# Optimization experiments

Hardware: AMD Instinct MI355X
Metric: run time of the kernel (lower is better)

Reference implementation:

```python
import jax, jax.numpy as jnp
import numpy as np
from jax.scipy.linalg import cholesky, solve_triangular, cho_solve

N, M, D = 16384, 2048, 8
VAR, LS = 1.0, 0.5      # RBF kernel hyperparameters (same for kernel_f and kernel_g)
JITTER = 1e-6
BATCH_RATE = 1.0
HALF_LOG_2PI = 0.5 * float(np.log(2.0 * np.pi))


def rbf(x1, x2):
    # K[i,j] = VAR * exp(-||x1_i - x2_j||^2 / (2 LS^2))
    d2 = (jnp.sum(x1 * x1, 1)[:, None] + jnp.sum(x2 * x2, 1)[None, :]
          - 2.0 * (x1 @ x2.T))
    return VAR * jnp.exp(-0.5 * d2 / (LS * LS))


def setup_inputs() -> dict:
    key = jax.random.key(0)
    ks = jax.random.split(key, 7)
    x = jax.random.normal(ks[0], (N, D), dtype=jnp.float32)
    y = jax.random.normal(ks[1], (N, 1), dtype=jnp.float32)
    z = 2.0 * jax.random.uniform(ks[2], (M, D), dtype=jnp.float32) - 1.0  # inducing inputs in [-1,1]^D
    q_m_f = 0.5 * jax.random.normal(ks[3], (M, 1), dtype=jnp.float32)
    q_m_g = 0.5 * jax.random.normal(ks[4], (M, 1), dtype=jnp.float32)
    # Cholesky-like params: identity plus small strictly-lower noise -> PD covariance
    q_L_f = jnp.eye(M, dtype=jnp.float32) + 0.01 * jnp.tril(
        jax.random.normal(ks[5], (M, M), dtype=jnp.float32), -1)
    q_L_g = jnp.eye(M, dtype=jnp.float32) + 0.01 * jnp.tril(
        jax.random.normal(ks[6], (M, M), dtype=jnp.float32), -1)
    return {"x": x, "y": y, "z": z, "q_m_f": q_m_f, "q_L_f": q_L_f,
            "q_m_g": q_m_g, "q_L_g": q_L_g}


def _gp_marginals_and_kl(x, z, q_m, q_L_raw):
    """Marginal posterior mean/var at x and KL(q(u)||p(u)) for one sparse GP."""
    L_S = jnp.tril(q_L_raw)                     # [M,M]
    Kuu = rbf(z, z) + JITTER * jnp.eye(M, dtype=x.dtype)
    Lk = cholesky(Kuu, lower=True)
    Kfu = rbf(x, z)                             # [N,M]
    # A = Kfu @ Kuu^{-1}
    A = cho_solve((Lk, True), Kfu.T).T          # [N,M]
    m = (A @ q_m)[:, 0]                         # [N]
    # diag(Kff + A (S - Kuu) A^T) = diag(Kff) + diag(A S A^T) - diag(Kfu A^T)
    S = L_S @ L_S.T
    diag_Kff = jnp.full((x.shape[0],), VAR, dtype=x.dtype)
    v = diag_Kff + jnp.sum((A @ S) * A, axis=1) - jnp.sum(A * Kfu, axis=1)
    # KL(N(q_m, S) || N(0, Kuu))
    alpha = solve_triangular(Lk, q_m, lower=True)       # Kuu^{-1/2} m
    W = solve_triangular(Lk, L_S, lower=True)           # Kuu^{-1/2} L_S
    logdet_K = 2.0 * jnp.sum(jnp.log(jnp.diag(Lk)))
    logdet_S = 2.0 * jnp.sum(jnp.log(jnp.abs(jnp.diag(L_S))))
    kl = 0.5 * (jnp.sum(W * W) + jnp.sum(alpha * alpha)
                - jnp.asarray(M, x.dtype) + logdet_K - logdet_S)
    return m, v, kl


def reference(x, y, z, q_m_f, q_L_f, q_m_g, q_L_g):
    m_f, v_f, kl_f = _gp_marginals_and_kl(x, z, q_m_f, q_L_f)
    m_g, v_g, kl_g = _gp_marginals_and_kl(x, z, q_m_g, q_L_g)
    yv = y[:, 0]
    # HetGaussian variational expectation (Saul et al. 2016):
    # E_q[log N(y | f, exp(g))] per point
    expectation = (-HALF_LOG_2PI - 0.5 * m_g
                   - 0.5 * ((yv - m_f) ** 2 + v_f) * jnp.exp(-m_g + 0.5 * v_g))
    elbo = BATCH_RATE * jnp.sum(expectation) - (kl_f + kl_g)
    return -elbo
```

## Files before the change

### kernel.cpp

```cpp
#include <hip/hip_runtime.h>
#include <math.h>

#define NN 16384
#define MM 2048
#define DD 8
#define NB 32
#define SZB ((size_t)16777216)

constexpr float HLOG2PI = 0.91893853320467274178f;

using short8  = __attribute__((ext_vector_type(8))) short;
using float4v = __attribute__((ext_vector_type(4))) float;

__device__ __forceinline__ float4v f4zero(){ float4v v; v[0]=0.f; v[1]=0.f; v[2]=0.f; v[3]=0.f; return v; }

__device__ __forceinline__ void bfsplit(float v, short& h, short& lo){
  unsigned b = __float_as_uint(v);
  h = (short)(b >> 16);
  float hf = __uint_as_float(b & 0xFFFF0000u);
  lo = (short)(__float_as_uint(v - hf) >> 16);
}
__device__ __forceinline__ float bf2f(short s){
  return __uint_as_float(((unsigned)(unsigned short)s) << 16);
}
__device__ __forceinline__ float4v mfma3(short8 ah, short8 al, short8 bh, short8 bl, float4v c){
  c = __builtin_amdgcn_mfma_f32_16x16x32_bf16(ah, bh, c, 0, 0, 0);
  c = __builtin_amdgcn_mfma_f32_16x16x32_bf16(ah, bl, c, 0, 0, 0);
  c = __builtin_amdgcn_mfma_f32_16x16x32_bf16(al, bh, c, 0, 0, 0);
  return c;
}

__device__ __forceinline__ float block_reduce(float v, float* scratch){
  int lane = threadIdx.x & 63;
  int w    = threadIdx.x >> 6;
  #pragma unroll
  for (int off=32; off; off>>=1) v += __shfl_down(v, off, 64);
  __syncthreads();
  if (lane==0) scratch[w] = v;
  __syncthreads();
  float r = 0.f;
  if (threadIdx.x < 4) r = scratch[threadIdx.x];
  if (w==0){ r += __shfl_down(r, 2, 64); r += __shfl_down(r, 1, 64); }
  return r;
}

__device__ __forceinline__ void stage64(float (*S)[68], const float* __restrict__ g, int ld, int t){
  #pragma unroll
  for (int p=t; p<1024; p+=256)
    *(float4*)&S[p>>4][(p&15)*4] = *(const float4*)&g[(size_t)(p>>4)*ld + (p&15)*4];
}
__device__ __forceinline__ void tile_gemm_step(float acc[4][4], const float (*As)[68], const float (*Bs)[68], int tx, int ty){
  for (int k=0;k<64;++k){
    float ar[4], bc4[4];
    #pragma unroll
    for (int u=0;u<4;++u){ ar[u]=As[ty*4+u][k]; bc4[u]=Bs[k][tx*4+u]; }
    #pragma unroll
    for (int u=0;u<4;++u)
      #pragma unroll
      for (int v=0;v<4;++v) acc[u][v] += ar[u]*bc4[v];
  }
}
__device__ __forceinline__ void tile_syrk_step(float acc[4][4], const float (*P)[68], const float (*Q)[68], int tx, int ty){
  for (int k=0;k<64;++k){
    float pr[4], qc[4];
    #pragma unroll
    for (int u=0;u<4;++u){ pr[u]=P[ty*4+u][k]; qc[u]=Q[tx*4+u][k]; }
    #pragma unroll
    for (int u=0;u<4;++u)
      #pragma unroll
      for (int v=0;v<4;++v) acc[u][v] += pr[u]*qc[v];
  }
}

__device__ __forceinline__ void factor64_reg(const float (*S)[68],
    float* __restrict__ lkd, float* __restrict__ sdg_, int d, int t){
  if (t < 64){
    float xr[64];
    #pragma unroll
    for (int c4=0;c4<16;++c4) *(float4*)&xr[c4*4] = *(const float4*)&S[t][c4*4];
    float myrp = 1.f;
    #pragma unroll
    for (int j=0;j<64;++j){
      float ajj = __shfl(xr[j], j, 64);
      float piv = sqrtf(fmaxf(ajj, 1e-20f));
      float rp  = 1.f/piv;
      float val = xr[j]*rp;
      if (t==j){ xr[j] = piv; myrp = rp; }
      else if (t>j) xr[j] = val;
      else val = 0.f;
      #pragma unroll
      for (int c=j+1;c<64;++c){
        float vc = __shfl(val, c, 64);
        if (c<=t) xr[c] -= val*vc;
      }
    }
    #pragma unroll
    for (int c=0;c<64;++c) if (c>t) xr[c] = 0.f;
    #pragma unroll
    for (int c4=0;c4<16;++c4)
      *(float4*)&lkd[d*4096 + t*64 + c4*4] = *(float4*)&xr[c4*4];
    sdg_[d*64 + t] = myrp;
  }
}


__global__ __launch_bounds__(256) void phase0_kernel(
    const float* __restrict__ z, float* __restrict__ kuu){
  __shared__ float As[64][68];
  __shared__ float Bs[64][68];
  const int t = threadIdx.x, tx = t & 15, ty = t >> 4;
  int idx = blockIdx.x;
  int r=0; while ((r+1)*(r+2)/2 <= idx) ++r;
  int c = idx - r*(r+1)/2;
  for (int p=t; p<128; p+=256){ int i=p>>1, h=p&1;
    *(float4*)&As[i][h*4] = *(const float4*)&z[(size_t)(r*64+i)*DD + h*4];
    *(float4*)&Bs[i][h*4] = *(const float4*)&z[(size_t)(c*64+i)*DD + h*4]; }
  __syncthreads();
  #pragma unroll
  for (int u=0;u<4;++u){
    float4 o;
    float* ov = (float*)&o;
    #pragma unroll
    for (int v=0;v<4;++v){
      float d2=0.f;
      #pragma unroll
      for (int d=0;d<8;++d){ float df=As[ty*4+u][d]-Bs[tx*4+v][d]; d2+=df*df; }
      float val = __expf(-2.f*d2);
      if (r*64+ty*4+u == c*64+tx*4+v) val += 1e-6f;
      ov[v] = val;
    }
    *(float4*)&kuu[(size_t)(r*64+ty*4+u)*MM + c*64 + tx*4] = o;
  }
}

__global__ __launch_bounds__(256) void diag0_kernel(
    const float* __restrict__ kuu, float* __restrict__ lkdiag, float* __restrict__ sdg){
  __shared__ float As[64][68];
  const int t = threadIdx.x;
  stage64(As, kuu, MM, t);
  __syncthreads();
  factor64_reg(As, lkdiag, sdg, 0, t);
}

__global__ __launch_bounds__(256) void panel_kernel(
    float* __restrict__ kuu, float* __restrict__ lkdiag,
    float* __restrict__ sdg, float* __restrict__ ltri, int kb){
  __shared__ float As[64][68];
  __shared__ float Bs[64][68];
  __shared__ float Cs[64][68];
  __shared__ float sd[64];
  const int t = threadIdx.x, tx = t & 15, ty = t >> 4;
  int idx = blockIdx.x;
  int r=0; while ((r+1)*(r+2)/2 <= idx) ++r;
  int c = idx - r*(r+1)/2;
  int bi = kb+1+r, bc = kb+1+c;
  stage64(Cs, lkdiag + kb*4096, 64, t);
  if (t < 64) sd[t] = sdg[kb*64 + t];
  stage64(As, kuu + (size_t)(bi*64)*MM + kb*64, MM, t);
  if (bc != bi) stage64(Bs, kuu + (size_t)(bc*64)*MM + kb*64, MM, t);
  __syncthreads();
  {
    int w = t>>6, l = t&63;
    if (w==0 || (w==1 && bc!=bi)){
      float (*S)[68] = (w==0)? As : Bs;
      float xr[64];
      #pragma unroll
      for (int c4=0;c4<16;++c4) *(float4*)&xr[c4*4] = *(const float4*)&S[l][c4*4];
      #pragma unroll
      for (int j=0;j<64;++j){
        float xj = xr[j]*sd[j];
        xr[j] = xj;
        #pragma unroll
        for (int cc=j+1;cc<64;++cc) xr[cc] -= xj*Cs[cc][j];
      }
      #pragma unroll
      for (int c4=0;c4<16;++c4) *(float4*)&S[l][c4*4] = *(float4*)&xr[c4*4];
    }
  }
  __syncthreads();
  if (bc == kb+1){
    for (int p=t;p<1024;p+=256)
      *(float4*)&ltri[(size_t)(bi*64+(p>>4))*MM + kb*64 + (p&15)*4] =
          *(float4*)&As[p>>4][(p&15)*4];
  }
  float acc[4][4] = {};
  tile_syrk_step(acc, As, (bc==bi)? As : Bs, tx, ty);
  if (bi==kb+1 && bc==kb+1){
    __syncthreads();
    #pragma unroll
    for (int u=0;u<4;++u)
      #pragma unroll
      for (int v=0;v<4;++v) Bs[ty*4+u][tx*4+v] = acc[u][v];
    __syncthreads();
    for (int p=t;p<1024;p+=256){
      int i=p>>4, c4=p&15;
      float4 kv = *(const float4*)&kuu[(size_t)(bi*64+i)*MM + bi*64 + c4*4];
      float4 bv = *(float4*)&Bs[i][c4*4];
      float4 o; o.x=kv.x-bv.x; o.y=kv.y-bv.y; o.z=kv.z-bv.z; o.w=kv.w-bv.w;
      *(float4*)&As[i][c4*4] = o;
    }
    __syncthreads();
    factor64_reg(As, lkdiag, sdg, kb+1, t);
  } else {
    #pragma unroll
    for (int u=0;u<4;++u){
      float4* dst = (float4*)&kuu[(size_t)(bi*64+ty*4+u)*MM + bc*64 + tx*4];
      float4 o = *dst;
      o.x-=acc[u][0]; o.y-=acc[u][1]; o.z-=acc[u][2]; o.w-=acc[u][3];
      *dst = o;
    }
  }
}

__global__ __launch_bounds__(256) void phase2_kernel(
    const float* __restrict__ lkdiag, float* __restrict__ linv){
  __shared__ float As[64][68];
  __shared__ float Bs[64][68];
  const int t = threadIdx.x, bid = blockIdx.x;
  stage64(As, lkdiag + bid*4096, 64, t);
  __syncthreads();
  if (t < 64){
    for (int j=0;j<64;++j){
      float s = (j==t)?1.f:0.f;
      for (int k=t;k<j;++k) s -= As[j][k]*Bs[k][t];
      Bs[j][t] = (j>=t)? s/As[j][j] : 0.f;
    }
  }
  __syncthreads();
  for (int p=t;p<1024;p+=256){ int i=p>>4, c4=p&15;
    *(float4*)&linv[(size_t)(bid*64+i)*MM + bid*64 + c4*4] = *(float4*)&Bs[i][c4*4]; }
}

__global__ __launch_bounds__(256) void p3l0_kernel(
    const float* __restrict__ ltri, float* __restrict__ linv){
  __shared__ float As[64][68];
  __shared__ float Bs[64][68];
  const int t = threadIdx.x, tx = t & 15, ty = t >> 4;
  int m = blockIdx.x;
  stage64(As, ltri + (size_t)((2*m+1)*64)*MM + (2*m)*64, MM, t);
  stage64(Bs, linv + (size_t)((2*m)*64)*MM   + (2*m)*64, MM, t);
  __syncthreads();
  float acc[4][4]={};
  tile_gemm_step(acc, As, Bs, tx, ty);
  __syncthreads();
  #pragma unroll
  for (int u=0;u<4;++u)
    #pragma unroll
    for (int v=0;v<4;++v) Bs[ty*4+u][tx*4+v] = acc[u][v];
  stage64(As, linv + (size_t)((2*m+1)*64)*MM + (2*m+1)*64, MM, t);
  __syncthreads();
  float o[4][4]={};
  tile_gemm_step(o, As, Bs, tx, ty);
  #pragma unroll
  for (int u=0;u<4;++u)
    *(float4*)&linv[(size_t)((2*m+1)*64+ty*4+u)*MM + (2*m)*64 + tx*4] =
        make_float4(-o[u][0],-o[u][1],-o[u][2],-o[u][3]);
}

__global__ __launch_bounds__(256) void p3l1_kernel(
    const float* __restrict__ ltri, float* __restrict__ linv, float* __restrict__ ptmp){
  __shared__ float As[64][68];
  __shared__ float Bs[64][68];
  const int t = threadIdx.x, tx = t & 15, ty = t >> 4;
  int m = blockIdx.x;
  float* pm = ptmp + (size_t)m*128*128;
  for (int ti=0; ti<2; ++ti)
    for (int tj=0; tj<2; ++tj){
      int rb = m*4 + 2 + ti, cb0 = m*4;
      float acc[4][4]={};
      for (int k=tj; k<2; ++k){
        __syncthreads();
        stage64(As, ltri + (size_t)(rb*64)*MM + (cb0+k)*64, MM, t);
        stage64(Bs, linv + (size_t)((cb0+k)*64)*MM + (cb0+tj)*64, MM, t);
        __syncthreads();
        tile_gemm_step(acc, As, Bs, tx, ty);
      }
      #pragma unroll
      for (int u=0;u<4;++u)
        *(float4*)&pm[(size_t)(ti*64+ty*4+u)*128 + tj*64 + tx*4] =
            make_float4(acc[u][0],acc[u][1],acc[u][2],acc[u][3]);
    }
  for (int ti=0; ti<2; ++ti)
    for (int tj=0; tj<2; ++tj){
      int rb = m*4 + 2 + ti;
      float acc[4][4]={};
      for (int k=0; k<=ti; ++k){
        __syncthreads();
        stage64(As, linv + (size_t)(rb*64)*MM + (m*4+2+k)*64, MM, t);
        stage64(Bs, pm + (size_t)(k*64)*128 + tj*64, 128, t);
        __syncthreads();
        tile_gemm_step(acc, As, Bs, tx, ty);
      }
      #pragma unroll
      for (int u=0;u<4;++u)
        *(float4*)&linv[(size_t)(rb*64+ty*4+u)*MM + (m*4+tj)*64 + tx*4] =
            make_float4(-acc[u][0],-acc[u][1],-acc[u][2],-acc[u][3]);
    }
}

__global__ __launch_bounds__(256) void p3lA_kernel(
    const float* __restrict__ ltri, const float* __restrict__ linv,
    float* __restrict__ ptmp, int s){
  __shared__ float As[64][68];
  __shared__ float Bs[64][68];
  const int t = threadIdx.x, tx = t & 15, ty = t >> 4;
  int nb = 1<<s, b = 64<<s;
  float* pmb = ptmp + (s==2 ? 131072 : (s==3 ? 393216 : 917504));
  int idx = blockIdx.x;
  int m = idx/(nb*nb), r2 = idx%(nb*nb);
  int ti = r2/nb, tj = r2%nb;
  int rb = m*2*nb + nb + ti, cb0 = m*2*nb;
  float acc[4][4]={};
  for (int k=tj; k<nb; ++k){
    __syncthreads();
    stage64(As, ltri + (size_t)(rb*64)*MM + (cb0+k)*64, MM, t);
    stage64(Bs, linv + (size_t)((cb0+k)*64)*MM + (cb0+tj)*64, MM, t);
    __syncthreads();
    tile_gemm_step(acc, As, Bs, tx, ty);
  }
  float* pm = pmb + (size_t)m*b*b;
  #pragma unroll
  for (int u=0;u<4;++u)
    *(float4*)&pm[(size_t)(ti*64+ty*4+u)*b + tj*64 + tx*4] =
        make_float4(acc[u][0],acc[u][1],acc[u][2],acc[u][3]);
}

__global__ __launch_bounds__(256) void p3lB_kernel(
    float* __restrict__ linv, const float* __restrict__ ptmp, int s){
  __shared__ float As[64][68];
  __shared__ float Bs[64][68];
  const int t = threadIdx.x, tx = t & 15, ty = t >> 4;
  int nb = 1<<s, b = 64<<s;
  const float* pmb = ptmp + (s==2 ? 131072 : (s==3 ? 393216 : 917504));
  int idx = blockIdx.x;
  int m = idx/(nb*nb), r2 = idx%(nb*nb);
  int ti = r2/nb, tj = r2%nb;
  int rb = m*2*nb + nb + ti;
  const float* pm = pmb + (size_t)m*b*b;
  float acc[4][4]={};
  for (int k=0; k<=ti; ++k){
    __syncthreads();
    stage64(As, linv + (size_t)(rb*64)*MM + (m*2*nb+nb+k)*64, MM, t);
    stage64(Bs, pm + (size_t)(k*64)*b + tj*64, b, t);
    __syncthreads();
    tile_gemm_step(acc, As, Bs, tx, ty);
  }
  #pragma unroll
  for (int u=0;u<4;++u)
    *(float4*)&linv[(size_t)(rb*64+ty*4+u)*MM + (m*2*nb+tj)*64 + tx*4] =
        make_float4(-acc[u][0],-acc[u][1],-acc[u][2],-acc[u][3]);
}

__global__ __launch_bounds__(256) void w_kernel(
    const float* __restrict__ linv, const float* __restrict__ qlf,
    const float* __restrict__ qlg, float* __restrict__ wf, float* __restrict__ wg){
  __shared__ float As[64][68];
  __shared__ float Bs[64][68];
  const int t = threadIdx.x, tx = t & 15, ty = t >> 4;
  int idx = blockIdx.x;
  int gp = idx/528, rem = idx%528;
  int bi=0; while ((bi+1)*(bi+2)/2 <= rem) ++bi;
  int bj = rem - bi*(bi+1)/2;
  const float* ql = gp ? qlg : qlf;
  float* w        = gp ? wg  : wf;
  float acc[4][4]={};
  for (int bk=bj; bk<=bi; ++bk){
    __syncthreads();
    stage64(As, linv + (size_t)(bi*64)*MM + bk*64, MM, t);
    stage64(Bs, ql   + (size_t)(bk*64)*MM + bj*64, MM, t);
    __syncthreads();
    if (bk==bj){
      for (int p=t;p<4096;p+=256){ int i=p>>6, c=p&63; if (i<c) Bs[i][c]=0.f; }
      __syncthreads();
    }
    tile_gemm_step(acc, As, Bs, tx, ty);
  }
  #pragma unroll
  for (int u=0;u<4;++u)
    *(float4*)&w[(size_t)(bi*64+ty*4+u)*MM + bj*64 + tx*4] =
        make_float4(acc[u][0],acc[u][1],acc[u][2],acc[u][3]);
}

__global__ __launch_bounds__(256) void alpha_kernel(
    const float* __restrict__ linv, const float* __restrict__ qmf,
    const float* __restrict__ qmg, float* __restrict__ af, float* __restrict__ ag){
  int t = threadIdx.x;
  int gw = blockIdx.x*4 + (t>>6), l = t&63;
  for (int job=gw; job<4096; job+=1024){
    int gp = job>>11, r = job&2047;
    const float* qm = gp ? qmg : qmf;
    float s=0.f;
    for (int c=l; c<=r; c+=64) s += linv[(size_t)r*MM+c]*qm[c];
    #pragma unroll
    for (int off=32; off; off>>=1) s += __shfl_down(s, off, 64);
    if (l==0) (gp ? ag : af)[r] = s;
  }
}


__global__ __launch_bounds__(256) void zfrag_kernel(const float* __restrict__ z,
    short* __restrict__ zfh, short* __restrict__ zfl, float* __restrict__ zn2){
  int zr = blockIdx.x*256 + threadIdx.x;
  float v[DD]; float s = 0.f;
  #pragma unroll
  for (int d=0; d<DD; ++d){ v[d] = z[zr*DD + d]; s += v[d]*v[d]; }
  zn2[zr] = s;
  size_t base = (size_t)(zr >> 4)*512 + (zr & 15)*32;
  #pragma unroll
  for (int k=0; k<32; ++k){
    short h = 0, lo = 0;
    if (k < DD) bfsplit(v[k], h, lo);
    zfh[base + k] = h; zfl[base + k] = lo;
  }
}

__global__ __launch_bounds__(256) void red_small(const float* __restrict__ lkd,
    const float* __restrict__ qlf, const float* __restrict__ qlg,
    const float* __restrict__ af, const float* __restrict__ ag,
    float* __restrict__ scal){
  __shared__ float scratch[4];
  float ldk=0, ldf=0, ldg=0, a2f=0, a2g=0;
  for (int i=threadIdx.x;i<MM;i+=256){
    int kb = i>>6, r = i&63;
    ldk += __logf(lkd[kb*4096 + r*64 + r]);
    ldf += __logf(fabsf(qlf[(size_t)i*MM+i]));
    ldg += __logf(fabsf(qlg[(size_t)i*MM+i]));
    float v = af[i]; a2f += v*v;
    v = ag[i];       a2g += v*v;
  }
  float r;
  r = block_reduce(ldk, scratch); if (threadIdx.x==0) scal[0] = 2.f*r;
  r = block_reduce(ldf, scratch); if (threadIdx.x==0) scal[1] = 2.f*r;
  r = block_reduce(ldg, scratch); if (threadIdx.x==0) scal[2] = 2.f*r;
  r = block_reduce(a2f, scratch); if (threadIdx.x==0) scal[3] = r;
  r = block_reduce(a2g, scratch); if (threadIdx.x==0) scal[4] = r;
}

__global__ __launch_bounds__(256) void redw_kernel(const float* __restrict__ wf,
    const float* __restrict__ wg, float* __restrict__ scal){
  __shared__ float scratch[4];
  size_t start  = (size_t)blockIdx.x*256 + threadIdx.x;
  size_t stride = (size_t)gridDim.x*256;
  float sf=0, sg=0;
  for (size_t p=start;p<(size_t)MM*MM;p+=stride){
    float v=wf[p]; sf += v*v;
    v=wg[p];       sg += v*v;
  }
  float r = block_reduce(sf, scratch);
  if (threadIdx.x==0) atomicAdd(&scal[5], r);
  r = block_reduce(sg, scratch);
  if (threadIdx.x==0) atomicAdd(&scal[6], r);
}

__global__ void kl_kernel(const float* __restrict__ scal, float* __restrict__ out){
  float klf = 0.5f*(scal[5] + scal[3] - (float)MM + scal[0] - scal[1]);
  float klg = 0.5f*(scal[6] + scal[4] - (float)MM + scal[0] - scal[2]);
  out[0] += klf + klg;
}

__global__ __launch_bounds__(256) void split_rowmajor(const float* __restrict__ src,
    short* __restrict__ dh, short* __restrict__ dl){
  int p = blockIdx.x*256 + threadIdx.x;
  int chunk = p >> 9, wi = p & 511;
  int mo = chunk >> 6, ko = chunk & 63;
  int row = mo*16 + (wi >> 5), col = ko*32 + (wi & 31);
  float v = src[(size_t)row*MM + col];
  short h, lo; bfsplit(v, h, lo);
  dh[p] = h; dl[p] = lo;
}

__global__ __launch_bounds__(256) void split_transpose(const float* __restrict__ src,
    short* __restrict__ dh, short* __restrict__ dl){
  __shared__ float tile[32][33];
  int t = threadIdx.x;
  int mb = blockIdx.x, kb = blockIdx.y;
  #pragma unroll
  for (int k=0;k<4;++k){
    int idx = t + k*256;
    int lr = idx >> 5, lc = idx & 31;
    tile[lr][lc] = src[(size_t)(kb*32+lr)*MM + mb*32 + lc];
  }
  __syncthreads();
  #pragma unroll
  for (int e=0;e<4;++e){
    int p = t*4 + e;
    int c = p >> 9, wi = p & 511;
    int i = (wi >> 5) & 15, kk = wi & 31;
    float v = tile[kk][c*16 + i];
    short h, lo; bfsplit(v, h, lo);
    size_t gp = ((size_t)(mb*2 + c)*64 + kb)*512 + wi;
    dh[gp] = h; dl[gp] = lo;
  }
}

__global__ __launch_bounds__(256, 2) void tt_mfma(
    const float* __restrict__ x, const float* __restrict__ zn2,
    const short* __restrict__ zfh, const short* __restrict__ zfl,
    const short* __restrict__ lvh, const short* __restrict__ lvl,
    short* __restrict__ tth, short* __restrict__ ttl){
  __shared__ __align__(16) short lAh[8192], lAl[8192], lBh[8192], lBl[8192];
  int t = threadIdx.x;
  int l = t & 63, w = t >> 6;
  int istrip = blockIdx.x, bj2 = blockIdx.y;
  int li = l & 15, q = l >> 4;
  int lofs = li*32 + q*8;
  int wn4 = (w>>1)*4, wm4 = (w&1)*4;

  short8 xh[2], xl[2];
  float xn2v[8];
  {
    float xn2t[2];
    #pragma unroll
    for (int tn=0; tn<2; ++tn){
      int n = istrip*128 + w*32 + tn*16 + li;
      const float4* xp = (const float4*)(x + (size_t)n*DD);
      float4 p0 = xp[0], p1 = xp[1];
      float v[8] = {p0.x,p0.y,p0.z,p0.w,p1.x,p1.y,p1.z,p1.w};
      float s = 0.f;
      #pragma unroll
      for (int d=0; d<8; ++d) s += v[d]*v[d];
      xn2t[tn] = s;
      short8 hh, ll;
      #pragma unroll
      for (int j=0; j<8; ++j){
        short h=0, lo=0;
        if (q==0) bfsplit(v[j], h, lo);
        hh[j]=h; ll[j]=lo;
      }
      xh[tn]=hh; xl[tn]=ll;
    }
    #pragma unroll
    for (int tn=0; tn<2; ++tn)
      #pragma unroll
      for (int r=0; r<4; ++r)
        xn2v[tn*4+r] = __shfl(xn2t[tn], q*4 + r, 64);
  }

  float4v acc[4][4];
  #pragma unroll
  for (int i=0;i<4;++i)
    #pragma unroll
    for (int j=0;j<4;++j) acc[i][j] = f4zero();

  int nkt = 2*bj2 + 2;
  for (int bk=0; bk<nkt; ++bk){
    __syncthreads();
    {
      short8 zh[4], zl[4];
      float zt2[4];
      #pragma unroll
      for (int tz=0; tz<4; ++tz){
        size_t zo = (size_t)(bk*4 + tz)*512 + lofs;
        zh[tz] = *(const short8*)(zfh + zo);
        zl[tz] = *(const short8*)(zfl + zo);
        zt2[tz] = zn2[bk*64 + tz*16 + li];
      }
      #pragma unroll
      for (int tn=0; tn<2; ++tn){
        #pragma unroll
        for (int tz=0; tz<4; ++tz){
          float4v s4 = mfma3(xh[tn], xl[tn], zh[tz], zl[tz], f4zero());
          #pragma unroll
          for (int r=0; r<4; ++r){
            float e = __expf(4.f*s4[r] - 2.f*(xn2v[tn*4+r] + zt2[tz]));
            short h, lo; bfsplit(e, h, lo);
            int pos = ((w*2+tn)*2 + (tz>>1))*512 + (q*4+r)*32 + (tz&1)*16 + li;
            lAh[pos] = h; lAl[pos] = lo;
          }
        }
      }
    }
    #pragma unroll
    for (int c4 = t; c4 < 1024; c4 += 256){
      int ch = c4 >> 6, wdi = c4 & 63;
      size_t g = ((size_t)(bj2*8 + (ch>>1))*64 + (size_t)(bk*2 + (ch&1)))*64 + wdi;
      ((uint4*)lBh)[c4] = ((const uint4*)lvh)[g];
      ((uint4*)lBl)[c4] = ((const uint4*)lvl)[g];
    }
    __syncthreads();
    #pragma unroll
    for (int s=0; s<2; ++s){
      short8 ah[4], al[4], bh[4], bl[4];
      #pragma unroll
      for (int tn=0; tn<4; ++tn){
        int off = ((wn4+tn)*2 + s)*512 + lofs;
        ah[tn] = *(const short8*)&lAh[off];
        al[tn] = *(const short8*)&lAl[off];
      }
      #pragma unroll
      for (int tm=0; tm<4; ++tm){
        int off = ((wm4+tm)*2 + s)*512 + lofs;
        bh[tm] = *(const short8*)&lBh[off];
        bl[tm] = *(const short8*)&lBl[off];
      }
      #pragma unroll
      for (int tn=0; tn<4; ++tn)
        #pragma unroll
        for (int tm=0; tm<4; ++tm)
          acc[tn][tm] = mfma3(ah[tn], al[tn], bh[tm], bl[tm], acc[tn][tm]);
    }
  }
  #pragma unroll
  for (int tn=0; tn<4; ++tn){
    int no_g = istrip*8 + wn4 + tn;
    #pragma unroll
    for (int tm=0; tm<4; ++tm){
      int mo_g = bj2*4 + (w&1)*2 + (tm>>1);
      size_t cb = ((size_t)no_g*64 + mo_g)*512;
      #pragma unroll
      for (int r=0; r<4; ++r){
        short h, lo; bfsplit(acc[tn][tm][r], h, lo);
        size_t pos = cb + (q*4+r)*32 + (tm&1)*16 + li;
        tth[pos] = h; ttl[pos] = lo;
      }
    }
  }
}

__global__ __launch_bounds__(256) void lin_v2(const short* __restrict__ tth,
    const short* __restrict__ ttl, const float* __restrict__ af, const float* __restrict__ ag,
    float* __restrict__ t2, float* __restrict__ lf, float* __restrict__ lg){
  int t = threadIdx.x;
  int w = t >> 6, l = t & 63;
  int n = blockIdx.x*4 + w;
  int g = l >> 2, j = l & 3;
  float s2=0.f, sf=0.f, sg=0.f;
  #pragma unroll
  for (int it=0; it<4; ++it){
    int ck = g + it*16;
    size_t off = ((size_t)(n>>4)*64 + ck)*512 + (n&15)*32 + j*8;
    short8 h8 = *(const short8*)(tth + off);
    short8 l8 = *(const short8*)(ttl + off);
    int m0 = ck*32 + j*8;
    float4 a0 = *(const float4*)(af + m0), a1 = *(const float4*)(af + m0 + 4);
    float4 g0 = *(const float4*)(ag + m0), g1 = *(const float4*)(ag + m0 + 4);
    float av[8] = {a0.x,a0.y,a0.z,a0.w,a1.x,a1.y,a1.z,a1.w};
    float gv[8] = {g0.x,g0.y,g0.z,g0.w,g1.x,g1.y,g1.z,g1.w};
    #pragma unroll
    for (int e=0; e<8; ++e){
      float tv = bf2f(h8[e]) + bf2f(l8[e]);
      s2 += tv*tv; sf += tv*av[e]; sg += tv*gv[e];
    }
  }
  #pragma unroll
  for (int off=32; off; off>>=1){
    s2 += __shfl_down(s2, off, 64);
    sf += __shfl_down(sf, off, 64);
    sg += __shfl_down(sg, off, 64);
  }
  if (l==0){ t2[n] = s2; lf[n] = sf; lg[n] = sg; }
}

__global__ __launch_bounds__(256, 2) void quad_mfma(
    const short* __restrict__ tth, const short* __restrict__ ttl,
    const short* __restrict__ wfh, const short* __restrict__ wfl,
    const short* __restrict__ wgh, const short* __restrict__ wgl,
    float* __restrict__ vfq, float* __restrict__ vgq){
  __shared__ __align__(16) short lAh[8192], lAl[8192], lBh[8192], lBl[8192];
  int t = threadIdx.x, l = t & 63, w = t >> 6;
  int istrip = blockIdx.x, bj2 = blockIdx.y;
  const short* gbh = blockIdx.z ? wgh : wfh;
  const short* gbl = blockIdx.z ? wgl : wfl;
  float* vq = blockIdx.z ? vgq : vfq;
  int li = l & 15, q = l >> 4;
  int lofs = li*32 + q*8;
  int wn4 = (w>>1)*4, wm4 = (w&1)*4;

  float4v acc[4][4];
  #pragma unroll
  for (int i=0;i<4;++i)
    #pragma unroll
    for (int j=0;j<4;++j) acc[i][j] = f4zero();

  for (int bk=2*bj2; bk<32; ++bk){
    __syncthreads();
    #pragma unroll
    for (int c4 = t; c4 < 1024; c4 += 256){
      int ch = c4 >> 6, wdi = c4 & 63;
      size_t ga = ((size_t)(istrip*8 + (ch>>1))*64 + (size_t)(bk*2 + (ch&1)))*64 + wdi;
      ((uint4*)lAh)[c4] = ((const uint4*)tth)[ga];
      ((uint4*)lAl)[c4] = ((const uint4*)ttl)[ga];
      size_t gb = ((size_t)(bj2*8 + (ch>>1))*64 + (size_t)(bk*2 + (ch&1)))*64 + wdi;
      ((uint4*)lBh)[c4] = ((const uint4*)gbh)[gb];
      ((uint4*)lBl)[c4] = ((const uint4*)gbl)[gb];
    }
    __syncthreads();
    #pragma unroll
    for (int s=0; s<2; ++s){
      short8 ah[4], al[4], bh[4], bl[4];
      #pragma unroll
      for (int tn=0; tn<4; ++tn){
        int off = ((wn4+tn)*2 + s)*512 + lofs;
        ah[tn] = *(const short8*)&lAh[off];
        al[tn] = *(const short8*)&lAl[off];
      }
      #pragma unroll
      for (int tm=0; tm<4; ++tm){
        int off = ((wm4+tm)*2 + s)*512 + lofs;
        bh[tm] = *(const short8*)&lBh[off];
        bl[tm] = *(const short8*)&lBl[off];
      }
      #pragma unroll
      for (int tn=0; tn<4; ++tn)
        #pragma unroll
        for (int tm=0; tm<4; ++tm)
          acc[tn][tm] = mfma3(ah[tn], al[tn], bh[tm], bl[tm], acc[tn][tm]);
    }
  }
  float rs[16];
  #pragma unroll
  for (int tn=0; tn<4; ++tn)
    #pragma unroll
    for (int r=0; r<4; ++r){
      float s = 0.f;
      #pragma unroll
      for (int tm=0; tm<4; ++tm){ float v = acc[tn][tm][r]; s += v*v; }
      rs[tn*4+r] = s;
    }
  #pragma unroll
  for (int off=8; off; off>>=1)
    #pragma unroll
    for (int k=0; k<16; ++k) rs[k] += __shfl_down(rs[k], off, 16);
  if (li == 0){
    #pragma unroll
    for (int tn=0; tn<4; ++tn)
      #pragma unroll
      for (int r=0; r<4; ++r){
        int n = istrip*128 + (w>>1)*64 + tn*16 + q*4 + r;
        atomicAdd(&vq[n], rs[tn*4+r]);
      }
  }
}

__global__ __launch_bounds__(256) void final_kernel(const float* __restrict__ y,
    const float* __restrict__ t2, const float* __restrict__ lf, const float* __restrict__ lg,
    const float* __restrict__ vfq, const float* __restrict__ vgq, float* __restrict__ out){
  __shared__ float scratch[4];
  int i = blockIdx.x*256 + threadIdx.x;
  float mf = lf[i], mg = lg[i];
  float vf = 1.f + vfq[i] - t2[i];
  float vg = 1.f + vgq[i] - t2[i];
  float dy = y[i] - mf;
  float e = -HLOG2PI - 0.5f*mg - 0.5f*(dy*dy + vf)*__expf(-mg + 0.5f*vg);
  float r = block_reduce(e, scratch);
  if (threadIdx.x==0) atomicAdd(out, -r);
}

extern "C" void kernel_launch(void* const* d_in, const int* in_sizes, int n_in,
                              void* d_out, int out_size, void* d_ws, size_t ws_size,
                              hipStream_t stream){
  (void)in_sizes; (void)n_in; (void)out_size; (void)ws_size;
  const float* x   = (const float*)d_in[0];
  const float* y   = (const float*)d_in[1];
  const float* z   = (const float*)d_in[2];
  const float* qmf = (const float*)d_in[3];
  const float* qlf = (const float*)d_in[4];
  const float* qmg = (const float*)d_in[5];
  const float* qlg = (const float*)d_in[6];
  float* out = (float*)d_out;
  char* Bw = (char*)d_ws;

  float* kuu  = (float*)Bw;
  float* linv = (float*)(Bw + SZB);
  float* wf   = (float*)(Bw + 2*SZB);
  float* wg   = (float*)(Bw + 3*SZB);
  short* lvh  = (short*)Bw;
  short* lvl  = (short*)(Bw + SZB/2);
  short* wfh  = (short*)(Bw + SZB);
  short* wfl  = (short*)(Bw + SZB + SZB/2);
  short* wgh  = (short*)(Bw + 2*SZB);
  short* wgl  = (short*)(Bw + 2*SZB + SZB/2);
  short* tth  = (short*)(Bw + 3*SZB);
  short* ttl  = (short*)(Bw + 3*SZB + (size_t)NN*MM*2);
  float* ltri   = (float*)(Bw + 4*SZB);
  float* ptmp   = (float*)(Bw + 5*SZB);
  float* lkdiag = (float*)(Bw + 5*SZB + (size_t)8388608);
  float* sdg    = (float*)(Bw + 5*SZB + (size_t)8388608 + (size_t)524288);
  float* sm   = (float*)(Bw + 3*SZB + (size_t)NN*MM*4);
  float* af = sm;          float* ag = af + MM;
  float* t2 = ag + MM;     float* lf = t2 + NN;   float* lg = lf + NN;
  float* vfq = lg + NN;    float* vgq = vfq + NN; float* scal = vgq + NN;
  float* zn2 = scal + 64 + 2048;
  short* zfh = (short*)(zn2 + MM);
  short* zfl = zfh + MM*32;

  hipMemsetAsync(out, 0, sizeof(float), stream);
  hipMemsetAsync(vfq, 0, (size_t)(2*NN + 64 + 2048)*sizeof(float), stream);
  hipMemsetAsync(wf,  0, 2*SZB, stream);
  hipMemsetAsync(linv,0, SZB,   stream);

  zfrag_kernel<<<MM/256, 256, 0, stream>>>(z, zfh, zfl, zn2);

  phase0_kernel<<<528, 256, 0, stream>>>(z, kuu);
  diag0_kernel<<<1, 256, 0, stream>>>(kuu, lkdiag, sdg);
  for (int kb = 0; kb < 31; ++kb){
    int T = NB - 1 - kb;
    panel_kernel<<<T*(T+1)/2, 256, 0, stream>>>(kuu, lkdiag, sdg, ltri, kb);
  }
  phase2_kernel<<<NB, 256, 0, stream>>>(lkdiag, linv);
  p3l0_kernel<<<16, 256, 0, stream>>>(ltri, linv);
  p3l1_kernel<<<8, 256, 0, stream>>>(ltri, linv, ptmp);
  for (int s = 2; s < 5; ++s){
    int nb = 1<<s, mc = 16>>s;
    p3lA_kernel<<<mc*nb*nb, 256, 0, stream>>>(ltri, linv, ptmp, s);
    p3lB_kernel<<<mc*nb*nb, 256, 0, stream>>>(linv, ptmp, s);
  }
  w_kernel<<<2*528, 256, 0, stream>>>(linv, qlf, qlg, wf, wg);
  alpha_kernel<<<256, 256, 0, stream>>>(linv, qmf, qmg, af, ag);

  red_small<<<1, 256, 0, stream>>>(lkdiag, qlf, qlg, af, ag, scal);
  redw_kernel<<<512, 256, 0, stream>>>(wf, wg, scal);
  kl_kernel<<<1, 1, 0, stream>>>(scal, out);

  split_rowmajor<<<MM*MM/256, 256, 0, stream>>>(linv, lvh, lvl);
  split_transpose<<<dim3(MM/32, MM/32), 256, 0, stream>>>(wf, wfh, wfl);
  split_transpose<<<dim3(MM/32, MM/32), 256, 0, stream>>>(wg, wgh, wgl);

  tt_mfma<<<dim3(NN/128, MM/128), 256, 0, stream>>>(x, zn2, zfh, zfl, lvh, lvl, tth, ttl);
  lin_v2<<<NN/4, 256, 0, stream>>>(tth, ttl, af, ag, t2, lf, lg);
  quad_mfma<<<dim3(NN/128, MM/128, 2), 256, 0, stream>>>(tth, ttl, wfh, wfl, wgh, wgl, vfq, vgq);
  final_kernel<<<NN/256, 256, 0, stream>>>(y, t2, lf, lg, vfq, vgq, out);
}
```

Before: 3.914 ms.

## Swizzle LDS tiles in MFMA GEMMs and merge split kernels into one launch

Measured after the change: 3.875 ms. Within noise of the previous version (-1.0%).

```diff
diff --git a/kernel.cpp b/kernel.cpp
--- a/kernel.cpp
+++ b/kernel.cpp
@@ -458,22 +458,31 @@
   out[0] += klf + klg;
 }
 
-__global__ __launch_bounds__(256) void split_rowmajor(const float* __restrict__ src,
-    short* __restrict__ dh, short* __restrict__ dl){
-  int p = blockIdx.x*256 + threadIdx.x;
-  int chunk = p >> 9, wi = p & 511;
-  int mo = chunk >> 6, ko = chunk & 63;
-  int row = mo*16 + (wi >> 5), col = ko*32 + (wi & 31);
-  float v = src[(size_t)row*MM + col];
-  short h, lo; bfsplit(v, h, lo);
-  dh[p] = h; dl[p] = lo;
-}
-
-__global__ __launch_bounds__(256) void split_transpose(const float* __restrict__ src,
-    short* __restrict__ dh, short* __restrict__ dl){
+__global__ __launch_bounds__(256) void split_all(
+    const float* __restrict__ linv, const float* __restrict__ wf,
+    const float* __restrict__ wg, short* __restrict__ lvh, short* __restrict__ lvl,
+    short* __restrict__ wfh, short* __restrict__ wfl,
+    short* __restrict__ wgh, short* __restrict__ wgl){
   __shared__ float tile[32][33];
-  int t = threadIdx.x;
-  int mb = blockIdx.x, kb = blockIdx.y;
+  const int t = threadIdx.x;
+  const int bid = blockIdx.x;
+  if (bid < 16384){
+    int p = bid*256 + t;
+    int chunk = p >> 9, wi = p & 511;
+    int mo = chunk >> 6, ko = chunk & 63;
+    int row = mo*16 + (wi >> 5), col = ko*32 + (wi & 31);
+    float v = linv[(size_t)row*MM + col];
+    short h, lo; bfsplit(v, h, lo);
+    lvh[p] = h; lvl[p] = lo;
+    return;
+  }
+  int idx2 = bid - 16384;
+  int zz = idx2 >> 12;
+  int rem = idx2 & 4095;
+  int mb = rem & 63, kb = rem >> 6;
+  const float* src = zz ? wg : wf;
+  short* dh = zz ? wgh : wfh;
+  short* dl = zz ? wgl : wfl;
   #pragma unroll
   for (int k=0;k<4;++k){
     int idx = t + k*256;
@@ -504,6 +513,7 @@
   int istrip = blockIdx.x, bj2 = blockIdx.y;
   int li = l & 15, q = l >> 4;
   int lofs = li*32 + q*8;
+  int lofs_s = li*32 + ((q ^ ((li>>1)&3)))*8;
   int wn4 = (w>>1)*4, wm4 = (w&1)*4;
 
   short8 xh[2], xl[2];
@@ -564,7 +574,9 @@
           for (int r=0; r<4; ++r){
             float e = __expf(4.f*s4[r] - 2.f*(xn2v[tn*4+r] + zt2[tz]));
             short h, lo; bfsplit(e, h, lo);
-            int pos = ((w*2+tn)*2 + (tz>>1))*512 + (q*4+r)*32 + (tz&1)*16 + li;
+            int rowc = q*4 + r;
+            int slot2 = (((tz&1)*2 + (li>>3)) ^ ((rowc>>1)&3));
+            int pos = ((w*2+tn)*2 + (tz>>1))*512 + rowc*32 + slot2*8 + (li&7);
             lAh[pos] = h; lAl[pos] = lo;
           }
         }
@@ -573,9 +585,11 @@
     #pragma unroll
     for (int c4 = t; c4 < 1024; c4 += 256){
       int ch = c4 >> 6, wdi = c4 & 63;
+      int wsw = (wdi & 60) | ((wdi ^ (wdi >> 3)) & 3);
+      int dst = ch*64 + wsw;
       size_t g = ((size_t)(bj2*8 + (ch>>1))*64 + (size_t)(bk*2 + (ch&1)))*64 + wdi;
-      ((uint4*)lBh)[c4] = ((const uint4*)lvh)[g];
-      ((uint4*)lBl)[c4] = ((const uint4*)lvl)[g];
+      ((uint4*)lBh)[dst] = ((const uint4*)lvh)[g];
+      ((uint4*)lBl)[dst] = ((const uint4*)lvl)[g];
     }
     __syncthreads();
     #pragma unroll
@@ -583,13 +597,13 @@
       short8 ah[4], al[4], bh[4], bl[4];
       #pragma unroll
       for (int tn=0; tn<4; ++tn){
-        int off = ((wn4+tn)*2 + s)*512 + lofs;
+        int off = ((wn4+tn)*2 + s)*512 + lofs_s;
         ah[tn] = *(const short8*)&lAh[off];
         al[tn] = *(const short8*)&lAl[off];
       }
       #pragma unroll
       for (int tm=0; tm<4; ++tm){
-        int off = ((wm4+tm)*2 + s)*512 + lofs;
+        int off = ((wm4+tm)*2 + s)*512 + lofs_s;
         bh[tm] = *(const short8*)&lBh[off];
         bl[tm] = *(const short8*)&lBl[off];
       }
@@ -663,7 +677,7 @@
   const short* gbl = blockIdx.z ? wgl : wfl;
   float* vq = blockIdx.z ? vgq : vfq;
   int li = l & 15, q = l >> 4;
-  int lofs = li*32 + q*8;
+  int lofs_s = li*32 + ((q ^ ((li>>1)&3)))*8;
   int wn4 = (w>>1)*4, wm4 = (w&1)*4;
 
   float4v acc[4][4];
@@ -677,12 +691,14 @@
     #pragma unroll
     for (int c4 = t; c4 < 1024; c4 += 256){
       int ch = c4 >> 6, wdi = c4 & 63;
+      int wsw = (wdi & 60) | ((wdi ^ (wdi >> 3)) & 3);
+      int dst = ch*64 + wsw;
       size_t ga = ((size_t)(istrip*8 + (ch>>1))*64 + (size_t)(bk*2 + (ch&1)))*64 + wdi;
-      ((uint4*)lAh)[c4] = ((const uint4*)tth)[ga];
-      ((uint4*)lAl)[c4] = ((const uint4*)ttl)[ga];
+      ((uint4*)lAh)[dst] = ((const uint4*)tth)[ga];
+      ((uint4*)lAl)[dst] = ((const uint4*)ttl)[ga];
       size_t gb = ((size_t)(bj2*8 + (ch>>1))*64 + (size_t)(bk*2 + (ch&1)))*64 + wdi;
-      ((uint4*)lBh)[c4] = ((const uint4*)gbh)[gb];
-      ((uint4*)lBl)[c4] = ((const uint4*)gbl)[gb];
+      ((uint4*)lBh)[dst] = ((const uint4*)gbh)[gb];
+      ((uint4*)lBl)[dst] = ((const uint4*)gbl)[gb];
     }
     __syncthreads();
     #pragma unroll
@@ -690,13 +706,13 @@
       short8 ah[4], al[4], bh[4], bl[4];
       #pragma unroll
       for (int tn=0; tn<4; ++tn){
-        int off = ((wn4+tn)*2 + s)*512 + lofs;
+        int off = ((wn4+tn)*2 + s)*512 + lofs_s;
         ah[tn] = *(const short8*)&lAh[off];
         al[tn] = *(const short8*)&lAl[off];
       }
       #pragma unroll
       for (int tm=0; tm<4; ++tm){
-        int off = ((wm4+tm)*2 + s)*512 + lofs;
+        int off = ((wm4+tm)*2 + s)*512 + lofs_s;
         bh[tm] = *(const short8*)&lBh[off];
         bl[tm] = *(const short8*)&lBl[off];
       }
@@ -812,9 +828,7 @@
   redw_kernel<<<512, 256, 0, stream>>>(wf, wg, scal);
   kl_kernel<<<1, 1, 0, stream>>>(scal, out);
 
-  split_rowmajor<<<MM*MM/256, 256, 0, stream>>>(linv, lvh, lvl);
-  split_transpose<<<dim3(MM/32, MM/32), 256, 0, stream>>>(wf, wfh, wfl);
-  split_transpose<<<dim3(MM/32, MM/32), 256, 0, stream>>>(wg, wgh, wgl);
+  split_all<<<24576, 256, 0, stream>>>(linv, wf, wg, lvh, lvl, wfh, wfl, wgh, wgl);
 
   tt_mfma<<<dim3(NN/128, MM/128), 256, 0, stream>>>(x, zn2, zfh, zfl, lvh, lvl, tth, ttl);
   lin_v2<<<NN/4, 256, 0, stream>>>(tth, ttl, af, ag, t2, lf, lg);
```
